# Performance work log

Measured on AMD Instinct MI355X. Metric: run time of the kernel, lower is better.

The kernel has to match this reference:

```python
import jax, jax.numpy as jnp
import numpy as np

NUM_GRAPHS = 256


def _gcn_norm(edge_index, num_nodes):
    # Add self-loops and compute symmetric normalization coeffs (PyG gcn_norm).
    loops = jnp.arange(num_nodes, dtype=edge_index.dtype)
    row = jnp.concatenate([edge_index[0], loops])  # source nodes
    col = jnp.concatenate([edge_index[1], loops])  # target nodes
    deg = jax.ops.segment_sum(jnp.ones_like(col, dtype=jnp.float32), col,
                              num_segments=num_nodes)
    dis = jnp.where(deg > 0, jax.lax.rsqrt(jnp.maximum(deg, 1.0)), 0.0)
    norm = dis[row] * dis[col]  # [E + N]
    return row, col, norm


def _gcn_conv(x, row, col, norm, W, b, num_nodes):
    h = x @ W                                        # [N, out] dense transform first
    msg = norm[:, None] * h[row]                     # gather + scale  [E+N, out]
    out = jax.ops.segment_sum(msg, col, num_segments=num_nodes)  # scatter-add
    return out + b


def setup_inputs() -> dict:
    key = jax.random.key(0)
    k = jax.random.split(key, 12)
    N, E, F_IN, H = 100000, 1600000, 64, 64
    x = jax.random.normal(k[0], (N, F_IN), dtype=jnp.float32)
    edge_index = jax.random.randint(k[1], (2, E), 0, N, dtype=jnp.int64)
    batch_index = jnp.sort(jax.random.randint(k[2], (N,), 0, NUM_GRAPHS, dtype=jnp.int64))
    s = 1.0 / np.sqrt(F_IN)
    W1 = jax.random.uniform(k[3], (F_IN, H), minval=-s, maxval=s, dtype=jnp.float32)
    b1 = jnp.zeros((H,), dtype=jnp.float32)
    W2 = jax.random.uniform(k[4], (H, H), minval=-s, maxval=s, dtype=jnp.float32)
    b2 = jnp.zeros((H,), dtype=jnp.float32)
    Wl1 = jax.random.uniform(k[5], (H, H // 2), minval=-s, maxval=s, dtype=jnp.float32)
    bl1 = jax.random.uniform(k[6], (H // 2,), minval=-s, maxval=s, dtype=jnp.float32)
    Wl2 = jax.random.uniform(k[7], (H // 2, 2), minval=-s, maxval=s, dtype=jnp.float32)
    bl2 = jax.random.uniform(k[8], (2,), minval=-s, maxval=s, dtype=jnp.float32)
    return {"x": x, "edge_index": edge_index, "batch_index": batch_index,
            "W1": W1, "b1": b1, "W2": W2, "b2": b2,
            "Wl1": Wl1, "bl1": bl1, "Wl2": Wl2, "bl2": bl2}


def reference(x, edge_index, batch_index, W1, b1, W2, b2, Wl1, bl1, Wl2, bl2):
    N = x.shape[0]
    row, col, norm = _gcn_norm(edge_index, N)
    h = jax.nn.relu(_gcn_conv(x, row, col, norm, W1, b1, N))
    h = jax.nn.relu(_gcn_conv(h, row, col, norm, W2, b2, N))
    # global mean pool over batch_index
    sums = jax.ops.segment_sum(h, batch_index, num_segments=NUM_GRAPHS)
    cnts = jax.ops.segment_sum(jnp.ones((N,), dtype=h.dtype), batch_index,
                               num_segments=NUM_GRAPHS)
    g = sums / jnp.maximum(cnts, 1.0)[:, None]       # [G, H]
    g = jax.nn.relu(g @ Wl1 + bl1)                    # dropout is identity in eval
    logits = g @ Wl2 + bl2
    return jax.nn.log_softmax(logits, axis=1)
```

## Files before the change

### kernel.cpp

```cpp
#include <hip/hip_runtime.h>
#include <hip/hip_fp8.h>
#include <cstdint>
#include <cstddef>


#define HF 64
#define BSH 8
#define BSZ 256
#define PCHUNK 4096
#define PADB 6144
#define CNTCLAMP (PADB - 4 * BSZ)
#define POISON 0xAAAAAAAAu
#define NG 256

typedef unsigned u32;
typedef unsigned v4u __attribute__((ext_vector_type(4)));
typedef float    v4f __attribute__((ext_vector_type(4)));

__device__ __forceinline__ unsigned short f2bf(float x) {
    unsigned u = __float_as_uint(x);
    unsigned r = (u + 0x7fffu + ((u >> 16) & 1u)) >> 16;
    return (unsigned short)r;
}
__device__ __forceinline__ float bfl(u32 w) { return __uint_as_float(w << 16); }
__device__ __forceinline__ float bfh(u32 w) { return __uint_as_float(w & 0xffff0000u); }

__device__ __forceinline__ u32 pack_fp8x4(float a, float b, float c, float d) {
#if __has_builtin(__builtin_amdgcn_cvt_pk_fp8_f32)
    int v = 0;
    v = __builtin_amdgcn_cvt_pk_fp8_f32(a, b, v, false);
    v = __builtin_amdgcn_cvt_pk_fp8_f32(c, d, v, true);
    return (u32)v;
#else
    __hip_fp8_e4m3 fa(a), fb(b), fc(c), fd(d);
    return (u32)fa.__x | ((u32)fb.__x << 8) | ((u32)fc.__x << 16) | ((u32)fd.__x << 24);
#endif
}
__device__ __forceinline__ void acc_fp8x4(float4& acc, u32 w) {
#if __has_builtin(__builtin_amdgcn_cvt_pk_f32_fp8)
    typedef float v2f __attribute__((ext_vector_type(2)));
    v2f lo = __builtin_amdgcn_cvt_pk_f32_fp8((int)w, false);
    v2f hi = __builtin_amdgcn_cvt_pk_f32_fp8((int)w, true);
    acc.x += lo[0]; acc.y += lo[1]; acc.z += hi[0]; acc.w += hi[1];
#else
    __hip_fp8_e4m3 a, b, c, d;
    a.__x = (unsigned char)(w);       b.__x = (unsigned char)(w >> 8);
    c.__x = (unsigned char)(w >> 16); d.__x = (unsigned char)(w >> 24);
    acc.x += (float)a; acc.y += (float)b; acc.z += (float)c; acc.w += (float)d;
#endif
}

__global__ __launch_bounds__(256) void k_part(const int* __restrict__ rows,
                                              const int* __restrict__ cols,
                                              u32* __restrict__ gcurb,
                                              u32* __restrict__ part, int E) {
    __shared__ u32 hist[512];
    __shared__ u32 off[512];
    __shared__ u32 obase[512];
    __shared__ u32 cur[512];
    __shared__ u32 sc[256];
    __shared__ u32 stage[PCHUNK];
    __shared__ unsigned short sbk[PCHUNK];
    const int tid = threadIdx.x;
    const int e0  = blockIdx.x * PCHUNK;
    u32 er[16], ec[16];

    hist[tid] = 0; hist[tid + 256] = 0;
    __syncthreads();
#pragma unroll
    for (int j = 0; j < 16; ++j) {
        int e = e0 + j * 256 + tid;
        if (e < E) {
            ec[j] = (u32)__builtin_nontemporal_load(cols + e);
            er[j] = (u32)__builtin_nontemporal_load(rows + e);
            atomicAdd(&hist[ec[j] >> BSH], 1u);
        } else ec[j] = 0xFFFFFFFFu;
    }
    __syncthreads();
    u32 c0 = hist[2 * tid], c1 = hist[2 * tid + 1];
    u32 s = c0 + c1;
    sc[tid] = s;
    __syncthreads();
    for (int o = 1; o < 256; o <<= 1) {
        u32 t = (tid >= o) ? sc[tid - o] : 0u;
        __syncthreads();
        sc[tid] += t;
        __syncthreads();
    }
    u32 ex = sc[tid] - s;
    off[2 * tid] = ex;          cur[2 * tid] = ex;
    off[2 * tid + 1] = ex + c0; cur[2 * tid + 1] = ex + c0;
    obase[2 * tid]     = c0 ? (atomicAdd(&gcurb[2 * tid], c0) - POISON) : 0u;
    obase[2 * tid + 1] = c1 ? (atomicAdd(&gcurb[2 * tid + 1], c1) - POISON) : 0u;
    __syncthreads();
#pragma unroll
    for (int j = 0; j < 16; ++j) {
        if (ec[j] != 0xFFFFFFFFu) {
            u32 bk  = ec[j] >> BSH;
            u32 pos = atomicAdd(&cur[bk], 1u);
            stage[pos] = ((ec[j] & (BSZ - 1)) << 17) | er[j];
            sbk[pos]   = (unsigned short)bk;
        }
    }
    __syncthreads();
    const int total = (e0 + PCHUNK <= E) ? PCHUNK : (E - e0);
    for (int i = tid; i < total; i += 256) {
        u32 bk = sbk[i];
        u32 pb = obase[bk] + ((u32)i - off[bk]);
        if (pb < PADB)
            part[(size_t)bk * PADB + pb] = stage[i];
    }
}

__global__ __launch_bounds__(256) void k_place2(const u32* __restrict__ gcurb,
                                                const u32* __restrict__ part,
                                                const float* __restrict__ x,
                                                u32* __restrict__ rowptr,
                                                float* __restrict__ dis,
                                                u32* __restrict__ s08,
                                                u32* __restrict__ h18,
                                                int* __restrict__ eidx,
                                                float* __restrict__ gm,
                                                int N, float S0) {
    __shared__ u32 cnt_[256];
    __shared__ u32 off_[257];
    __shared__ u32 sc[256];
    __shared__ u32 cur[256];
    __shared__ u32 outb[PADB];
    const int tid = threadIdx.x;
    const int b   = blockIdx.x;
    const int n0  = b << BSH;
    const u32 base = (u32)b * PADB;
    u32 cntB = gcurb[b] - POISON; if (cntB > CNTCLAMP) cntB = CNTCLAMP;

    if (b == 0 && tid < 16) {
        s08[(size_t)N * 16 + tid] = 0u;
        h18[(size_t)N * 16 + tid] = 0u;
    }
    if (b == 0) {
        for (int i = tid; i < NG * HF; i += 256) gm[i] = 0.f;
    }

    cnt_[tid] = 0;
    __syncthreads();
    for (u32 i = tid; i < cntB; i += 256)
        atomicAdd(&cnt_[part[base + i] >> 17], 1u);
    __syncthreads();
    u32 v  = cnt_[tid];
    bool live = (n0 + tid) < N;
    u32 vs = v + 1u;
    u32 p  = live ? ((vs + 3u) & ~3u) : 0u;
    sc[tid] = p;
    __syncthreads();
    for (int o = 1; o < 256; o <<= 1) {
        u32 t = (tid >= o) ? sc[tid - o] : 0u;
        __syncthreads();
        sc[tid] += t;
        __syncthreads();
    }
    u32 ex = sc[tid] - p;
    off_[tid] = ex; cur[tid] = ex;
    if (tid == 255) off_[256] = sc[255];
    __syncthreads();
    const u32 cntP = off_[256];
    if (live) {
        u32 dg = vs; if (dg > 1023u) dg = 1023u;
        rowptr[n0 + tid] = (base + ex) | (dg << 22);
        dis[n0 + tid]    = rsqrtf(1.0f + (float)v);
    }
    {
        int nmax = min(256, N - n0);
        for (int idx = tid; idx < nmax * 16; idx += 256) {
            int nl = idx >> 4, f4 = idx & 15;
            float d  = S0 * rsqrtf(1.0f + (float)cnt_[nl]);
            v4f xv = __builtin_nontemporal_load(
                (const v4f*)(x + (size_t)(n0 + nl) * HF) + f4);
            s08[(size_t)(n0 + nl) * 16 + f4] =
                pack_fp8x4(d * xv[0], d * xv[1], d * xv[2], d * xv[3]);
        }
    }
    for (u32 i = tid; i < cntP; i += 256) outb[i] = (u32)N;
    __syncthreads();
    for (u32 i = tid; i < cntB; i += 256) {
        u32 pv  = part[base + i];
        u32 pos = atomicAdd(&cur[pv >> 17], 1u);
        outb[pos] = pv & 0x1FFFFu;
    }
    __syncthreads();
    if (live) outb[cur[tid]] = (u32)tid;
    __syncthreads();
    for (u32 i = tid; i < cntP; i += 256)
        eidx[base + i] = (int)outb[i];
}

template <int OUTFP8>
__global__ __launch_bounds__(512, 8) void k_gtrans(const u32* __restrict__ rowptr,
                                                   const int* __restrict__ eidx,
                                                   const u32* __restrict__ hs8,
                                                   const float* __restrict__ W,
                                                   const float* __restrict__ dis,
                                                   const float* __restrict__ bias,
                                                   u32* __restrict__ OUT8,
                                                   float* __restrict__ gm,
                                                   const int* __restrict__ batch,
                                                   int N, float invS, float outS) {
    __shared__ float ws[64 * 64];
    __shared__ u32 xs2[128 * 34];
    __shared__ int   sbg[128];
    __shared__ float pool[128];
    const int tid  = threadIdx.x;
    const int row0 = blockIdx.x * 128;

    if constexpr (!OUTFP8) {
        if (tid < 128) {
            int r = row0 + tid;
            sbg[tid]  = (r < N) ? batch[r] : -1;
            pool[tid] = 0.f;
        }
    }

#pragma unroll
    for (int i = 0; i < 2; ++i) {
        int idx4 = i * 512 + tid;
        *(float4*)&ws[idx4 * 4] = ((const float4*)W)[idx4];
    }

    const int qq = tid >> 4;
    const int f4 = tid & 15;
    const int nb0 = row0 + qq * 4;
    v4u rp4 = *(const v4u*)(rowptr + nb0);
#pragma unroll 1
    for (int j = 0; j < 4; ++j) {
        const int nl = qq * 4 + j;
        const int n  = row0 + nl;
        float4 acc = float4{0.f, 0.f, 0.f, 0.f};
        if (n < N) {
            u32 rp    = rp4[j];
            u32 start = rp & 0x3FFFFFu;
            int ngr   = (int)(((rp >> 22) + 3u) >> 2);
            const v4u* eb = (const v4u*)(eidx + start);
            int g = 0;
            for (; g + 1 < ngr; g += 2) {
                v4u ea  = eb[g];
                v4u eb2 = eb[g + 1];
                u32 wa0 = hs8[(size_t)ea[0] * 16 + f4];
                u32 wa1 = hs8[(size_t)ea[1] * 16 + f4];
                u32 wa2 = hs8[(size_t)ea[2] * 16 + f4];
                u32 wa3 = hs8[(size_t)ea[3] * 16 + f4];
                u32 wb0 = hs8[(size_t)eb2[0] * 16 + f4];
                u32 wb1 = hs8[(size_t)eb2[1] * 16 + f4];
                u32 wb2 = hs8[(size_t)eb2[2] * 16 + f4];
                u32 wb3 = hs8[(size_t)eb2[3] * 16 + f4];
                acc_fp8x4(acc, wa0); acc_fp8x4(acc, wa1);
                acc_fp8x4(acc, wa2); acc_fp8x4(acc, wa3);
                acc_fp8x4(acc, wb0); acc_fp8x4(acc, wb1);
                acc_fp8x4(acc, wb2); acc_fp8x4(acc, wb3);
            }
            if (g < ngr) {
                v4u ea = eb[g];
                u32 w0 = hs8[(size_t)ea[0] * 16 + f4];
                u32 w1 = hs8[(size_t)ea[1] * 16 + f4];
                u32 w2 = hs8[(size_t)ea[2] * 16 + f4];
                u32 w3 = hs8[(size_t)ea[3] * 16 + f4];
                acc_fp8x4(acc, w0); acc_fp8x4(acc, w1);
                acc_fp8x4(acc, w2); acc_fp8x4(acc, w3);
            }
        }
        u32 lo = (u32)f2bf(acc.x) | ((u32)f2bf(acc.y) << 16);
        u32 hi = (u32)f2bf(acc.z) | ((u32)f2bf(acc.w) << 16);
        xs2[nl * 34 + f4 * 2]     = lo;
        xs2[nl * 34 + f4 * 2 + 1] = hi;
    }
    __syncthreads();

    const int rg = tid >> 4;
    const int cg = tid & 15;
    float4 a0 = float4{0.f, 0.f, 0.f, 0.f};
    float4 a1 = a0, a2 = a0, a3 = a0;

#pragma unroll 4
    for (int k2 = 0; k2 < 32; ++k2) {
        float4 wv0 = *(float4*)&ws[(2 * k2)     * 64 + cg * 4];
        float4 wv1 = *(float4*)&ws[(2 * k2 + 1) * 64 + cg * 4];
        u32 p0 = xs2[(rg * 4 + 0) * 34 + k2];
        u32 p1 = xs2[(rg * 4 + 1) * 34 + k2];
        u32 p2 = xs2[(rg * 4 + 2) * 34 + k2];
        u32 p3 = xs2[(rg * 4 + 3) * 34 + k2];
        float x0e = bfl(p0), x0o = bfh(p0);
        float x1e = bfl(p1), x1o = bfh(p1);
        float x2e = bfl(p2), x2o = bfh(p2);
        float x3e = bfl(p3), x3o = bfh(p3);
        a0.x += x0e * wv0.x; a0.y += x0e * wv0.y; a0.z += x0e * wv0.z; a0.w += x0e * wv0.w;
        a1.x += x1e * wv0.x; a1.y += x1e * wv0.y; a1.z += x1e * wv0.z; a1.w += x1e * wv0.w;
        a2.x += x2e * wv0.x; a2.y += x2e * wv0.y; a2.z += x2e * wv0.z; a2.w += x2e * wv0.w;
        a3.x += x3e * wv0.x; a3.y += x3e * wv0.y; a3.z += x3e * wv0.z; a3.w += x3e * wv0.w;
        a0.x += x0o * wv1.x; a0.y += x0o * wv1.y; a0.z += x0o * wv1.z; a0.w += x0o * wv1.w;
        a1.x += x1o * wv1.x; a1.y += x1o * wv1.y; a1.z += x1o * wv1.z; a1.w += x1o * wv1.w;
        a2.x += x2o * wv1.x; a2.y += x2o * wv1.y; a2.z += x2o * wv1.z; a2.w += x2o * wv1.w;
        a3.x += x3o * wv1.x; a3.y += x3o * wv1.y; a3.z += x3o * wv1.z; a3.w += x3o * wv1.w;
    }

    float4 bv = ((const float4*)bias)[cg];
    float4 accs[4] = {a0, a1, a2, a3};
    if constexpr (OUTFP8) {
#pragma unroll
        for (int j = 0; j < 4; ++j) {
            int row = row0 + rg * 4 + j;
            if (row < N) {
                float d  = dis[row];
                float dd = d * invS;
                float4 a = accs[j];
                a.x = fmaxf(dd * a.x + bv.x, 0.f);
                a.y = fmaxf(dd * a.y + bv.y, 0.f);
                a.z = fmaxf(dd * a.z + bv.z, 0.f);
                a.w = fmaxf(dd * a.w + bv.w, 0.f);
                float so = d * outS;
                OUT8[(size_t)row * 16 + cg] =
                    pack_fp8x4(so * a.x, so * a.y, so * a.z, so * a.w);
            }
        }
    } else {
        const int g0s = sbg[0];
        float4 ps0 = float4{0.f, 0.f, 0.f, 0.f};
        float4 ps1 = ps0;
        bool any1 = false;
#pragma unroll
        for (int j = 0; j < 4; ++j) {
            int rl  = rg * 4 + j;
            int row = row0 + rl;
            if (row < N) {
                float d  = dis[row];
                float dd = d * invS;
                float4 a = accs[j];
                a.x = fmaxf(dd * a.x + bv.x, 0.f);
                a.y = fmaxf(dd * a.y + bv.y, 0.f);
                a.z = fmaxf(dd * a.z + bv.z, 0.f);
                a.w = fmaxf(dd * a.w + bv.w, 0.f);
                if (sbg[rl] == g0s) {
                    ps0.x += a.x; ps0.y += a.y; ps0.z += a.z; ps0.w += a.w;
                } else {
                    ps1.x += a.x; ps1.y += a.y; ps1.z += a.z; ps1.w += a.w;
                    any1 = true;
                }
            }
        }
        atomicAdd(&pool[cg * 4 + 0], ps0.x);
        atomicAdd(&pool[cg * 4 + 1], ps0.y);
        atomicAdd(&pool[cg * 4 + 2], ps0.z);
        atomicAdd(&pool[cg * 4 + 3], ps0.w);
        if (any1) {
            atomicAdd(&pool[64 + cg * 4 + 0], ps1.x);
            atomicAdd(&pool[64 + cg * 4 + 1], ps1.y);
            atomicAdd(&pool[64 + cg * 4 + 2], ps1.z);
            atomicAdd(&pool[64 + cg * 4 + 3], ps1.w);
        }
        __syncthreads();
        int lastv = N - 1 - row0; if (lastv > 127) lastv = 127;
        const int g1s = sbg[lastv];
        if (tid < 64) {
            atomicAdd(&gm[g0s * HF + tid], pool[tid]);
        } else if (tid < 128 && g1s != g0s) {
            atomicAdd(&gm[g1s * HF + (tid - 64)], pool[tid]);
        }
    }
}

__device__ __forceinline__ int lower_bound(const int* __restrict__ a, int n, int key) {
    int lo = 0, hi = n;
    while (lo < hi) { int mid = (lo + hi) >> 1; if (a[mid] < key) lo = mid + 1; else hi = mid; }
    return lo;
}

__global__ __launch_bounds__(64) void k_head(const float* __restrict__ gm,
                                             const int* __restrict__ batch,
                                             const float* __restrict__ Wl1,
                                             const float* __restrict__ bl1,
                                             const float* __restrict__ Wl2,
                                             const float* __restrict__ bl2,
                                             float* __restrict__ out, int N) {
    __shared__ float gml[64];
    const int g    = blockIdx.x;
    const int lane = threadIdx.x;
    int s = lower_bound(batch, N, g);
    int e = lower_bound(batch, N, g + 1);
    gml[lane] = gm[g * HF + lane] / fmaxf((float)(e - s), 1.0f);
    __syncthreads();
    if (lane < 32) {
        float a = bl1[lane];
#pragma unroll
        for (int k = 0; k < 64; ++k) a += gml[k] * Wl1[k * 32 + lane];
        a = fmaxf(a, 0.f);
        float l0 = a * Wl2[2 * lane];
        float l1 = a * Wl2[2 * lane + 1];
#pragma unroll
        for (int o = 1; o < 32; o <<= 1) {
            l0 += __shfl_xor(l0, o);
            l1 += __shfl_xor(l1, o);
        }
        if (lane == 0) {
            l0 += bl2[0]; l1 += bl2[1];
            float m   = fmaxf(l0, l1);
            float lse = m + logf(expf(l0 - m) + expf(l1 - m));
            out[2 * g]     = l0 - lse;
            out[2 * g + 1] = l1 - lse;
        }
    }
}

extern "C" void kernel_launch(void* const* d_in, const int* in_sizes, int n_in,
                              void* d_out, int out_size, void* d_ws, size_t ws_size,
                              hipStream_t stream) {
    const float* x   = (const float*)d_in[0];
    const int*   ei  = (const int*)d_in[1];
    const int*   bi  = (const int*)d_in[2];
    const float* W1  = (const float*)d_in[3];
    const float* b1  = (const float*)d_in[4];
    const float* W2  = (const float*)d_in[5];
    const float* b2  = (const float*)d_in[6];
    const float* Wl1 = (const float*)d_in[7];
    const float* bl1 = (const float*)d_in[8];
    const float* Wl2 = (const float*)d_in[9];
    const float* bl2 = (const float*)d_in[10];
    float* out = (float*)d_out;

    const int N = in_sizes[0] / HF;
    const int E = in_sizes[1] / 2;
    const int* rows = ei;
    const int* cols = ei + E;
    const int NB = (N + BSZ - 1) / BSZ;
    const size_t EP = (size_t)NB * PADB;

    const float S0 = 4.0f, S1 = 16.0f;

    float* ws = (float*)d_ws;
    size_t o = 0;
    float* dis    = ws + o; o += ((size_t)N + 63) / 64 * 64;
    u32*   A8     = (u32*)(ws + o); o += (size_t)(N + 1) * 16;
    u32*   B8     = (u32*)(ws + o); o += (size_t)(N + 1) * 16;
    u32*   rowptr = (u32*)(ws + o); o += ((size_t)N + 63) / 64 * 64;
    u32*   part   = (u32*)(ws + o); o += EP;
    int*   eidx   = (int*)(ws + o); o += EP;
    u32*   gcurb  = (u32*)(ws + o); o += 512;
    float* gm     = ws + o; o += (size_t)NG * HF;

    const int tb = (N + 127) / 128;

    k_part<<<(E + PCHUNK - 1) / PCHUNK, 256, 0, stream>>>(rows, cols, gcurb, part, E);
    k_place2<<<NB, 256, 0, stream>>>(gcurb, part, x, rowptr, dis, A8, B8, eidx, gm, N, S0);

    k_gtrans<1><<<tb, 512, 0, stream>>>(rowptr, eidx, A8, W1, dis, b1, B8, gm, bi,
                                        N, 1.0f / S0, S1);
    k_gtrans<0><<<tb, 512, 0, stream>>>(rowptr, eidx, B8, W2, dis, b2, nullptr, gm, bi,
                                        N, 1.0f / S1, 0.f);

    k_head<<<NG, 64, 0, stream>>>(gm, bi, Wl1, bl1, Wl2, bl2, out, N);
}
```

Measured before the change: 229.5 us.

## Replace bucketed two-pass CSR build with per-node atomic count and scatter

Replaces the LDS-staged bucket partition (k_part plus k_place2) with three simple kernels: a global atomic degree count per target node, a per-block scan that writes rowptr, dis, cursors, self-loop slot and fp8 input, and a global-atomic scatter of source indices into CSR slots. This drops the intermediate partition buffer and its extra read and write pass. In exchange it adds 3.2M global atomics on random addresses and scattered 4-byte stores, and edge order within a row becomes nondeterministic. It also relies on the degree array being pre-poisoned with POISON, and degrees are clamped at 1022.

```diff
diff --git a/kernel.cpp b/kernel.cpp
--- a/kernel.cpp
+++ b/kernel.cpp
@@ -7,9 +7,7 @@
 #define HF 64
 #define BSH 8
 #define BSZ 256
-#define PCHUNK 4096
 #define PADB 6144
-#define CNTCLAMP (PADB - 4 * BSZ)
 #define POISON 0xAAAAAAAAu
 #define NG 256
 
@@ -50,147 +48,86 @@
 #endif
 }
 
-__global__ __launch_bounds__(256) void k_part(const int* __restrict__ rows,
-                                              const int* __restrict__ cols,
-                                              u32* __restrict__ gcurb,
-                                              u32* __restrict__ part, int E) {
-    __shared__ u32 hist[512];
-    __shared__ u32 off[512];
-    __shared__ u32 obase[512];
-    __shared__ u32 cur[512];
+__global__ __launch_bounds__(256) void k_count(const int* __restrict__ cols,
+                                               u32* __restrict__ degP,
+                                               u32* __restrict__ s08,
+                                               u32* __restrict__ h18,
+                                               float* __restrict__ gm,
+                                               int N, int E) {
+    const int tid = threadIdx.x;
+    if (blockIdx.x == 0) {
+        if (tid < 16) {
+            s08[(size_t)N * 16 + tid] = 0u;
+            h18[(size_t)N * 16 + tid] = 0u;
+        }
+        for (int i = tid; i < NG * HF; i += 256) gm[i] = 0.f;
+    }
+    const int stride = gridDim.x * 256;
+    for (int e = blockIdx.x * 256 + tid; e < E; e += stride)
+        atomicAdd(&degP[(u32)cols[e]], 1u);
+}
+
+__global__ __launch_bounds__(256) void k_nodes(const u32* __restrict__ degP,
+                                               const float* __restrict__ x,
+                                               u32* __restrict__ rowptr,
+                                               float* __restrict__ dis,
+                                               u32* __restrict__ cur,
+                                               u32* __restrict__ s08,
+                                               int* __restrict__ eidx,
+                                               int N, int NB, float S0) {
     __shared__ u32 sc[256];
-    __shared__ u32 stage[PCHUNK];
-    __shared__ unsigned short sbk[PCHUNK];
-    const int tid = threadIdx.x;
-    const int e0  = blockIdx.x * PCHUNK;
-    u32 er[16], ec[16];
-
-    hist[tid] = 0; hist[tid + 256] = 0;
-    __syncthreads();
-#pragma unroll
-    for (int j = 0; j < 16; ++j) {
-        int e = e0 + j * 256 + tid;
-        if (e < E) {
-            ec[j] = (u32)__builtin_nontemporal_load(cols + e);
-            er[j] = (u32)__builtin_nontemporal_load(rows + e);
-            atomicAdd(&hist[ec[j] >> BSH], 1u);
-        } else ec[j] = 0xFFFFFFFFu;
-    }
-    __syncthreads();
-    u32 c0 = hist[2 * tid], c1 = hist[2 * tid + 1];
-    u32 s = c0 + c1;
-    sc[tid] = s;
-    __syncthreads();
-    for (int o = 1; o < 256; o <<= 1) {
-        u32 t = (tid >= o) ? sc[tid - o] : 0u;
-        __syncthreads();
-        sc[tid] += t;
-        __syncthreads();
-    }
-    u32 ex = sc[tid] - s;
-    off[2 * tid] = ex;          cur[2 * tid] = ex;
-    off[2 * tid + 1] = ex + c0; cur[2 * tid + 1] = ex + c0;
-    obase[2 * tid]     = c0 ? (atomicAdd(&gcurb[2 * tid], c0) - POISON) : 0u;
-    obase[2 * tid + 1] = c1 ? (atomicAdd(&gcurb[2 * tid + 1], c1) - POISON) : 0u;
-    __syncthreads();
-#pragma unroll
-    for (int j = 0; j < 16; ++j) {
-        if (ec[j] != 0xFFFFFFFFu) {
-            u32 bk  = ec[j] >> BSH;
-            u32 pos = atomicAdd(&cur[bk], 1u);
-            stage[pos] = ((ec[j] & (BSZ - 1)) << 17) | er[j];
-            sbk[pos]   = (unsigned short)bk;
-        }
-    }
-    __syncthreads();
-    const int total = (e0 + PCHUNK <= E) ? PCHUNK : (E - e0);
-    for (int i = tid; i < total; i += 256) {
-        u32 bk = sbk[i];
-        u32 pb = obase[bk] + ((u32)i - off[bk]);
-        if (pb < PADB)
-            part[(size_t)bk * PADB + pb] = stage[i];
-    }
-}
-
-__global__ __launch_bounds__(256) void k_place2(const u32* __restrict__ gcurb,
-                                                const u32* __restrict__ part,
-                                                const float* __restrict__ x,
-                                                u32* __restrict__ rowptr,
-                                                float* __restrict__ dis,
-                                                u32* __restrict__ s08,
-                                                u32* __restrict__ h18,
-                                                int* __restrict__ eidx,
-                                                float* __restrict__ gm,
-                                                int N, float S0) {
-    __shared__ u32 cnt_[256];
-    __shared__ u32 off_[257];
-    __shared__ u32 sc[256];
-    __shared__ u32 cur[256];
-    __shared__ u32 outb[PADB];
     const int tid = threadIdx.x;
     const int b   = blockIdx.x;
-    const int n0  = b << BSH;
-    const u32 base = (u32)b * PADB;
-    u32 cntB = gcurb[b] - POISON; if (cntB > CNTCLAMP) cntB = CNTCLAMP;
-
-    if (b == 0 && tid < 16) {
-        s08[(size_t)N * 16 + tid] = 0u;
-        h18[(size_t)N * 16 + tid] = 0u;
-    }
-    if (b == 0) {
-        for (int i = tid; i < NG * HF; i += 256) gm[i] = 0.f;
-    }
-
-    cnt_[tid] = 0;
-    __syncthreads();
-    for (u32 i = tid; i < cntB; i += 256)
-        atomicAdd(&cnt_[part[base + i] >> 17], 1u);
-    __syncthreads();
-    u32 v  = cnt_[tid];
-    bool live = (n0 + tid) < N;
-    u32 vs = v + 1u;
-    u32 p  = live ? ((vs + 3u) & ~3u) : 0u;
-    sc[tid] = p;
-    __syncthreads();
-    for (int o = 1; o < 256; o <<= 1) {
-        u32 t = (tid >= o) ? sc[tid - o] : 0u;
+
+    if (b < NB) {
+        const int n0 = b << BSH;
+        bool live = (n0 + tid) < N;
+        u32 v = live ? (degP[n0 + tid] - POISON) : 0u;
+        if (v > 1022u) v = 1022u;
+        u32 p = live ? ((v + 1u + 3u) & ~3u) : 0u;
+        sc[tid] = p;
         __syncthreads();
-        sc[tid] += t;
-        __syncthreads();
-    }
-    u32 ex = sc[tid] - p;
-    off_[tid] = ex; cur[tid] = ex;
-    if (tid == 255) off_[256] = sc[255];
-    __syncthreads();
-    const u32 cntP = off_[256];
-    if (live) {
-        u32 dg = vs; if (dg > 1023u) dg = 1023u;
-        rowptr[n0 + tid] = (base + ex) | (dg << 22);
-        dis[n0 + tid]    = rsqrtf(1.0f + (float)v);
-    }
-    {
-        int nmax = min(256, N - n0);
-        for (int idx = tid; idx < nmax * 16; idx += 256) {
-            int nl = idx >> 4, f4 = idx & 15;
-            float d  = S0 * rsqrtf(1.0f + (float)cnt_[nl]);
-            v4f xv = __builtin_nontemporal_load(
-                (const v4f*)(x + (size_t)(n0 + nl) * HF) + f4);
-            s08[(size_t)(n0 + nl) * 16 + f4] =
-                pack_fp8x4(d * xv[0], d * xv[1], d * xv[2], d * xv[3]);
-        }
-    }
-    for (u32 i = tid; i < cntP; i += 256) outb[i] = (u32)N;
-    __syncthreads();
-    for (u32 i = tid; i < cntB; i += 256) {
-        u32 pv  = part[base + i];
-        u32 pos = atomicAdd(&cur[pv >> 17], 1u);
-        outb[pos] = pv & 0x1FFFFu;
-    }
-    __syncthreads();
-    if (live) outb[cur[tid]] = (u32)tid;
-    __syncthreads();
-    for (u32 i = tid; i < cntP; i += 256)
-        eidx[base + i] = (int)outb[i];
+        for (int o = 1; o < 256; o <<= 1) {
+            u32 t = (tid >= o) ? sc[tid - o] : 0u;
+            __syncthreads();
+            sc[tid] += t;
+            __syncthreads();
+        }
+        if (live) {
+            u32 ex    = sc[tid] - p;
+            u32 start = (u32)b * PADB + ex;
+            rowptr[n0 + tid] = start | ((v + 1u) << 22);
+            dis[n0 + tid]    = rsqrtf(1.0f + (float)v);
+            cur[n0 + tid]    = start;
+            eidx[start + v]  = n0 + tid;
+            for (u32 q = v + 1u; q < p; ++q)
+                eidx[start + q] = N;
+        }
+    }
+    const int stride = gridDim.x * 256;
+    for (int idx = b * 256 + tid; idx < N * 16; idx += stride) {
+        int n = idx >> 4, f4 = idx & 15;
+        u32 dv = degP[n] - POISON; if (dv > 1022u) dv = 1022u;
+        float d = S0 * rsqrtf(1.0f + (float)dv);
+        v4f xv = __builtin_nontemporal_load(
+            (const v4f*)(x + (size_t)n * HF) + f4);
+        s08[(size_t)n * 16 + f4] =
+            pack_fp8x4(d * xv[0], d * xv[1], d * xv[2], d * xv[3]);
+    }
+}
+
+__global__ __launch_bounds__(256) void k_scatter(const int* __restrict__ rows,
+                                                 const int* __restrict__ cols,
+                                                 u32* __restrict__ cur,
+                                                 int* __restrict__ eidx, int E) {
+    const int tid = threadIdx.x;
+    const int stride = gridDim.x * 256;
+    for (int e = blockIdx.x * 256 + tid; e < E; e += stride) {
+        int r = rows[e];
+        int c = cols[e];
+        u32 pos = atomicAdd(&cur[(u32)c], 1u);
+        eidx[pos] = r;
+    }
 }
 
 template <int OUTFP8>
@@ -437,16 +374,17 @@
     float* dis    = ws + o; o += ((size_t)N + 63) / 64 * 64;
     u32*   A8     = (u32*)(ws + o); o += (size_t)(N + 1) * 16;
     u32*   B8     = (u32*)(ws + o); o += (size_t)(N + 1) * 16;
-    u32*   rowptr = (u32*)(ws + o); o += ((size_t)N + 63) / 64 * 64;
-    u32*   part   = (u32*)(ws + o); o += EP;
+    u32*   rowptr = (u32*)(ws + o); o += ((size_t)N + 127) / 64 * 64;
+    u32*   degP   = (u32*)(ws + o); o += ((size_t)N + 63) / 64 * 64;
+    u32*   cur    = (u32*)(ws + o); o += ((size_t)N + 63) / 64 * 64;
     int*   eidx   = (int*)(ws + o); o += EP;
-    u32*   gcurb  = (u32*)(ws + o); o += 512;
     float* gm     = ws + o; o += (size_t)NG * HF;
 
     const int tb = (N + 127) / 128;
 
-    k_part<<<(E + PCHUNK - 1) / PCHUNK, 256, 0, stream>>>(rows, cols, gcurb, part, E);
-    k_place2<<<NB, 256, 0, stream>>>(gcurb, part, x, rowptr, dis, A8, B8, eidx, gm, N, S0);
+    k_count<<<2048, 256, 0, stream>>>(cols, degP, A8, B8, gm, N, E);
+    k_nodes<<<2048, 256, 0, stream>>>(degP, x, rowptr, dis, cur, A8, eidx, N, NB, S0);
+    k_scatter<<<2048, 256, 0, stream>>>(rows, cols, cur, eidx, E);
 
     k_gtrans<1><<<tb, 512, 0, stream>>>(rowptr, eidx, A8, W1, dis, b1, B8, gm, bi,
                                         N, 1.0f / S0, S1);
```

Result: slower. 383.6 us (+67.2%).
